# Kernel tuning notes

Measured on AMD Instinct MI355X. Metric: run time of the kernel, lower is better.

Reference implementation:

```python
import jax, jax.numpy as jnp
import numpy as np

B, T, S, D, V = 8, 64, 512, 512, 50000


def setup_inputs() -> dict:
    key = jax.random.key(0)
    k1, k2, k3, k4, k5 = jax.random.split(key, 5)
    x = jax.random.normal(k1, (B, T, D), dtype=jnp.float32)
    attn_dist = jax.random.normal(k2, (B, T, S), dtype=jnp.float32)
    enc_batch_extend_vocab = jax.random.randint(k3, (B, S), 0, V, dtype=jnp.int64)
    W_proj = jax.random.normal(k4, (D, V), dtype=jnp.float32) * (1.0 / np.sqrt(D))
    b_proj = jnp.zeros((V,), dtype=jnp.float32)
    W_pgen = jax.random.normal(k5, (D, 1), dtype=jnp.float32) * (1.0 / np.sqrt(D))
    b_pgen = jnp.zeros((1,), dtype=jnp.float32)
    return {"x": x, "attn_dist": attn_dist,
            "enc_batch_extend_vocab": enc_batch_extend_vocab,
            "W_proj": W_proj, "b_proj": b_proj,
            "W_pgen": W_pgen, "b_pgen": b_pgen}


def reference(x, attn_dist, enc_batch_extend_vocab, W_proj, b_proj, W_pgen, b_pgen):
    # pointer-generator head, temp=1, beam_search=False
    temp = 1.0
    # p_gen gate: [B, T, 1]
    alpha = jax.nn.sigmoid(jnp.einsum('btd,de->bte', x, W_pgen) + b_pgen)
    # vocab projection + softmax: [B, T, V]
    logit = jnp.einsum('btd,dv->btv', x, W_proj) + b_proj
    vocab_dist = jax.nn.softmax(logit / temp, axis=2)
    vocab_dist_ = alpha * vocab_dist
    # copy distribution over source positions: [B, T, S]
    attn = jax.nn.softmax(attn_dist / temp, axis=-1)
    attn_ = (1.0 - alpha) * attn
    # scatter_add copy probs into vocab dim (index broadcast over T)
    b_idx = jnp.arange(B)[:, None, None]        # [B,1,1]
    t_idx = jnp.arange(T)[None, :, None]        # [1,T,1]
    v_idx = enc_batch_extend_vocab[:, None, :]  # [B,1,S]
    merged = vocab_dist_.at[b_idx, t_idx, v_idx].add(attn_)
    return jnp.log(merged)
```

## Files before the change

kernel.cpp:

```cpp
#include <hip/hip_runtime.h>
#include <math.h>
#include <stdint.h>

#define B_ 8
#define T_ 64
#define S_ 512
#define D_ 512
#define V_ 50000
#define VP_ 50176
#define M_ (B_*T_)
#define ROWB_ ((size_t)V_ * 4)

typedef __bf16 bf16_t;
typedef bf16_t bf16x8 __attribute__((ext_vector_type(8)));
typedef float  f32x4  __attribute__((ext_vector_type(4)));

__device__ inline float blk_sum(float v, float* sm) {
    #pragma unroll
    for (int o = 32; o > 0; o >>= 1) v += __shfl_down(v, o);
    int lane = threadIdx.x & 63, wid = threadIdx.x >> 6;
    __syncthreads();
    if (lane == 0) sm[wid] = v;
    __syncthreads();
    return sm[0] + sm[1] + sm[2] + sm[3];
}

__device__ inline float blk_max(float v, float* sm) {
    #pragma unroll
    for (int o = 32; o > 0; o >>= 1) v = fmaxf(v, __shfl_down(v, o));
    int lane = threadIdx.x & 63, wid = threadIdx.x >> 6;
    __syncthreads();
    if (lane == 0) sm[wid] = v;
    __syncthreads();
    return fmaxf(fmaxf(sm[0], sm[1]), fmaxf(sm[2], sm[3]));
}

__device__ inline void unpack8(uint4 u, float f[8]) {
    uint32_t w0 = u.x, w1 = u.y, w2 = u.z, w3 = u.w;
    f[0] = __uint_as_float(w0 << 16); f[1] = __uint_as_float(w0 & 0xffff0000u);
    f[2] = __uint_as_float(w1 << 16); f[3] = __uint_as_float(w1 & 0xffff0000u);
    f[4] = __uint_as_float(w2 << 16); f[5] = __uint_as_float(w2 & 0xffff0000u);
    f[6] = __uint_as_float(w3 << 16); f[7] = __uint_as_float(w3 & 0xffff0000u);
}

#define CONVB_ (784 * 8)

__global__ __launch_bounds__(256) void kprep(
    const float* __restrict__ W, bf16_t* __restrict__ Wt,
    const float* __restrict__ x, const float* __restrict__ attn_dist,
    const float* __restrict__ W_pgen, const float* __restrict__ b_pgen,
    float* __restrict__ logalpha_out, float* __restrict__ attn_out, bf16_t* __restrict__ xb,
    const int* __restrict__ idx, int* __restrict__ owner_g)
{
    __shared__ float tile[64][65];
    int bid = blockIdx.x;
    int tid = threadIdx.x;

    if (bid < CONVB_) {
        int v0 = (bid % 784) * 64;
        int k0 = (bid / 784) * 64;
        #pragma unroll
        for (int p = 0; p < 4; p++) {
            int kl = (tid >> 4) + p * 16;
            int v  = v0 + (tid & 15) * 4;
            float4 val = make_float4(0.f, 0.f, 0.f, 0.f);
            if (v < V_)
                val = *reinterpret_cast<const float4*>(&W[(size_t)(k0 + kl) * V_ + v]);
            tile[kl][(tid & 15) * 4 + 0] = val.x;
            tile[kl][(tid & 15) * 4 + 1] = val.y;
            tile[kl][(tid & 15) * 4 + 2] = val.z;
            tile[kl][(tid & 15) * 4 + 3] = val.w;
        }
        __syncthreads();
        #pragma unroll
        for (int p = 0; p < 2; p++) {
            int vl = (tid >> 3) + p * 32;
            int kc = (tid & 7) * 8;
            union { bf16_t h[8]; uint4 u; } pk;
            #pragma unroll
            for (int j = 0; j < 8; j++) pk.h[j] = (bf16_t)tile[kc + j][vl];
            *reinterpret_cast<uint4*>(&Wt[(size_t)(v0 + vl) * D_ + k0 + kc]) = pk.u;
        }
    } else if (bid < CONVB_ + M_) {
        float* sm = &tile[0][0];
        int row = bid - CONVB_;

        float2 xv = reinterpret_cast<const float2*>(x + (size_t)row * D_)[tid];
        float2 wv = reinterpret_cast<const float2*>(W_pgen)[tid];
        union { bf16_t h[2]; uint32_t u; } pk;
        pk.h[0] = (bf16_t)xv.x; pk.h[1] = (bf16_t)xv.y;
        reinterpret_cast<uint32_t*>(xb + (size_t)row * D_)[tid] = pk.u;

        float dot = blk_sum(xv.x * wv.x + xv.y * wv.y, sm);
        float alpha = 1.f / (1.f + expf(-(dot + b_pgen[0])));
        if (tid == 0) logalpha_out[row] = logf(alpha);

        float a0 = attn_dist[(size_t)row * S_ + tid];
        float a1 = attn_dist[(size_t)row * S_ + tid + 256];
        float mx = blk_max(fmaxf(a0, a1), sm);
        float e0 = expf(a0 - mx), e1 = expf(a1 - mx);
        float s = blk_sum(e0 + e1, sm);
        float scale = (1.f - alpha) / s;
        attn_out[(size_t)row * S_ + tid]       = e0 * scale;
        attn_out[(size_t)row * S_ + tid + 256] = e1 * scale;
    } else {
        int* ids = reinterpret_cast<int*>(&tile[0][0]);
        int b = bid - (CONVB_ + M_);
        for (int s = tid; s < S_; s += 256) ids[s] = idx[b * S_ + s];
        __syncthreads();
        for (int s = tid; s < S_; s += 256) {
            int v = ids[s], o = s;
            for (int s2 = 0; s2 < s; s2++) if (ids[s2] == v) { o = s2; break; }
            owner_g[b * S_ + s] = o;
        }
    }
}

#define GBM 128
#define GBN 128
#define GBK 32
#define NT2_ (D_/GBK)

__global__ __launch_bounds__(256) void k2_mfma(
    const bf16_t* __restrict__ A, const bf16_t* __restrict__ Wt,
    const float* __restrict__ bias, char* __restrict__ outB)
{
    __shared__ bf16_t As0[GBM][GBK], As1[GBM][GBK];
    __shared__ bf16_t Bs0[GBN][GBK], Bs1[GBN][GBK];
    int tid  = threadIdx.x;
    int lane = tid & 63;
    int w    = tid >> 6;
    int wm   = w >> 1, wn = w & 1;
    int bn = blockIdx.x * GBN;
    int bm = blockIdx.y * GBM;

    f32x4 acc[4][4] = {};

#define STAGE(dstA, dstB, k0)                                                          \
    {                                                                                  \
        _Pragma("unroll")                                                              \
        for (int i = 0; i < 2; i++) {                                                  \
            int e = (w * 2 + i) * 512 + lane * 8;                                      \
            int r = e >> 5, c = e & 31;                                                \
            __builtin_amdgcn_global_load_lds(                                          \
                (const __attribute__((address_space(1))) void*)                        \
                    &A[(size_t)(bm + r) * D_ + (k0) + c],                              \
                (__attribute__((address_space(3))) void*)&dstA[(w * 2 + i) * 16][0],   \
                16, 0, 0);                                                             \
            __builtin_amdgcn_global_load_lds(                                          \
                (const __attribute__((address_space(1))) void*)                        \
                    &Wt[(size_t)(bn + r) * D_ + (k0) + c],                             \
                (__attribute__((address_space(3))) void*)&dstB[(w * 2 + i) * 16][0],   \
                16, 0, 0);                                                             \
        }                                                                              \
    }

#define COMPUTE(srcA, srcB)                                                            \
    {                                                                                  \
        bf16x8 af[4], bfr[4];                                                          \
        int kb = (lane >> 4) * 8;                                                      \
        _Pragma("unroll")                                                              \
        for (int mi = 0; mi < 4; mi++)                                                 \
            af[mi] = *reinterpret_cast<const bf16x8*>(&srcA[wm * 64 + mi * 16 + (lane & 15)][kb]); \
        _Pragma("unroll")                                                              \
        for (int ni = 0; ni < 4; ni++)                                                 \
            bfr[ni] = *reinterpret_cast<const bf16x8*>(&srcB[wn * 64 + ni * 16 + (lane & 15)][kb]); \
        _Pragma("unroll")                                                              \
        for (int mi = 0; mi < 4; mi++)                                                 \
            _Pragma("unroll")                                                          \
            for (int ni = 0; ni < 4; ni++)                                             \
                acc[mi][ni] = __builtin_amdgcn_mfma_f32_16x16x32_bf16(af[mi], bfr[ni], acc[mi][ni], 0, 0, 0); \
    }

    STAGE(As0, Bs0, 0);
    asm volatile("s_waitcnt vmcnt(0)" ::: "memory");
    __syncthreads();

    #pragma unroll
    for (int tt = 0; tt < NT2_ / 2; tt++) {
        int k0 = tt * 2 * GBK;
        if (k0 + GBK < D_) STAGE(As1, Bs1, k0 + GBK);
        COMPUTE(As0, Bs0);
        asm volatile("s_waitcnt vmcnt(0)" ::: "memory");
        __syncthreads();
        if (k0 + 2 * GBK < D_) STAGE(As0, Bs0, k0 + 2 * GBK);
        COMPUTE(As1, Bs1);
        asm volatile("s_waitcnt vmcnt(0)" ::: "memory");
        __syncthreads();
    }
#undef STAGE
#undef COMPUTE

    int cm = bm + wm * 64, cn = bn + wn * 64;
    #pragma unroll
    for (int ni = 0; ni < 4; ni++) {
        int n = cn + ni * 16 + (lane & 15);
        float bv = (n < V_) ? bias[n] : 0.f;
        #pragma unroll
        for (int mi = 0; mi < 4; mi++) {
            int rbase = cm + mi * 16 + (lane >> 4) * 4;
            #pragma unroll
            for (int r = 0; r < 4; r++) {
                bf16_t val = (bf16_t)(acc[mi][ni][r] + bv);
                *reinterpret_cast<bf16_t*>(outB + (size_t)(rbase + r) * ROWB_ + 2 * (size_t)n) = val;
            }
        }
    }
}

#define CHUNK_ 2048
#define NCH_ ((V_ + CHUNK_ - 1) / CHUNK_)

__global__ __launch_bounds__(256) void k345_final(
    char* __restrict__ outB, const float* __restrict__ attn_, const int* __restrict__ idx,
    const int* __restrict__ owner_g, const float* __restrict__ logalpha)
{
    __shared__ float att[S_];
    __shared__ int own[S_], ids[S_];
    __shared__ float smm[4], sms[4];
    int row = blockIdx.x;
    int b = row >> 6;
    int tid = threadIdx.x;
    int lane = tid & 63, wid = tid >> 6;

    for (int s = tid; s < S_; s += 256) {
        att[s] = attn_[(size_t)row * S_ + s];
        own[s] = owner_g[b * S_ + s];
        ids[s] = idx[b * S_ + s];
    }

    const uint4* L4 = reinterpret_cast<const uint4*>(outB + (size_t)row * ROWB_);
    float m = -INFINITY, se = 0.f;
    for (int i = tid; i < V_ / 8; i += 256) {
        uint4 u = L4[i];
        float f[8]; unpack8(u, f);
        float m8 = fmaxf(fmaxf(fmaxf(f[0], f[1]), fmaxf(f[2], f[3])),
                         fmaxf(fmaxf(f[4], f[5]), fmaxf(f[6], f[7])));
        float mn = fmaxf(m, m8);
        se = se * __expf(m - mn)
           + __expf(f[0] - mn) + __expf(f[1] - mn) + __expf(f[2] - mn) + __expf(f[3] - mn)
           + __expf(f[4] - mn) + __expf(f[5] - mn) + __expf(f[6] - mn) + __expf(f[7] - mn);
        m = mn;
    }
    #pragma unroll
    for (int o = 32; o > 0; o >>= 1) {
        float m2 = __shfl_down(m, o);
        float s2 = __shfl_down(se, o);
        float mn = fmaxf(m, m2);
        if (mn == -INFINITY) { se = 0.f; }
        else se = se * __expf(m - mn) + s2 * __expf(m2 - mn);
        m = mn;
    }
    __syncthreads();
    if (lane == 0) { smm[wid] = m; sms[wid] = se; }
    __syncthreads();
    float M = smm[0], Ssum = sms[0];
    #pragma unroll
    for (int wv = 1; wv < 4; wv++) {
        float m2 = smm[wv], s2 = sms[wv];
        float mn = fmaxf(M, m2);
        if (mn != -INFINITY) Ssum = Ssum * __expf(M - mn) + s2 * __expf(m2 - mn);
        M = mn;
    }
    float logden = M + logf(Ssum);
    float c_ = logalpha[row] - logden;

    for (int s = tid; s < S_; s += 256)
        if (own[s] != s) atomicAdd(&att[own[s]], att[s]);
    __syncthreads();

    const ushort* Lrow = reinterpret_cast<const ushort*>(outB + (size_t)row * ROWB_);
    float* frow = reinterpret_cast<float*>(outB + (size_t)row * ROWB_);
    for (int c = NCH_ - 1; c >= 0; c--) {
        int i0 = c * CHUNK_ + tid * 8;
        uint4 u = make_uint4(0, 0, 0, 0);
        bool act = (i0 + 8 <= V_);
        if (act) u = *reinterpret_cast<const uint4*>(Lrow + i0);
        __syncthreads();
        if (act) {
            float f[8]; unpack8(u, f);
            float4 lo = make_float4(f[0] + c_, f[1] + c_, f[2] + c_, f[3] + c_);
            float4 hi = make_float4(f[4] + c_, f[5] + c_, f[6] + c_, f[7] + c_);
            *reinterpret_cast<float4*>(frow + i0)     = lo;
            *reinterpret_cast<float4*>(frow + i0 + 4) = hi;
        }
        __syncthreads();
    }

    for (int s = tid; s < S_; s += 256) {
        if (own[s] == s) {
            int v = ids[s];
            frow[v] = logf(expf(frow[v]) + att[s]);
        }
    }
}

__global__ __launch_bounds__(256) void k1_alpha_attn(
    const float* __restrict__ x, const float* __restrict__ attn_dist,
    const float* __restrict__ W_pgen, const float* __restrict__ b_pgen,
    float* __restrict__ logalpha_out, float* __restrict__ attn_out)
{
    __shared__ float sm[4];
    int row = blockIdx.x;
    int tid = threadIdx.x;
    float2 xv = reinterpret_cast<const float2*>(x + (size_t)row * D_)[tid];
    float2 wv = reinterpret_cast<const float2*>(W_pgen)[tid];
    float dot = blk_sum(xv.x * wv.x + xv.y * wv.y, sm);
    float alpha = 1.f / (1.f + expf(-(dot + b_pgen[0])));
    if (tid == 0) logalpha_out[row] = logf(alpha);
    float a0 = attn_dist[(size_t)row * S_ + tid];
    float a1 = attn_dist[(size_t)row * S_ + tid + 256];
    float mx = blk_max(fmaxf(a0, a1), sm);
    float e0 = expf(a0 - mx), e1 = expf(a1 - mx);
    float s = blk_sum(e0 + e1, sm);
    float scale = (1.f - alpha) / s;
    attn_out[(size_t)row * S_ + tid]       = e0 * scale;
    attn_out[(size_t)row * S_ + tid + 256] = e1 * scale;
}

__global__ __launch_bounds__(512) void k5a_owner(const int* __restrict__ idx, int* __restrict__ owner_g)
{
    __shared__ int ids[S_];
    int b = blockIdx.x;
    int s = threadIdx.x;
    ids[s] = idx[b * S_ + s];
    __syncthreads();
    int v = ids[s], o = s;
    for (int s2 = 0; s2 < s; s2++) if (ids[s2] == v) { o = s2; break; }
    owner_g[b * S_ + s] = o;
}

#define BM 64
#define BN 64
#define BK 16
__global__ __launch_bounds__(256) void k2_gemm(
    const float* __restrict__ A, const float* __restrict__ W,
    const float* __restrict__ bias, float* __restrict__ C)
{
    __shared__ float As2[BK][BM + 1];
    __shared__ float Bs2[BK][BN + 1];
    int bn = blockIdx.x * BN;
    int bm = blockIdx.y * BM;
    int tid = threadIdx.x;
    int tx = tid & 15;
    int ty = tid >> 4;
    bool full_n = (bn + BN <= V_);
    float acc[4][4] = {};
    for (int k0 = 0; k0 < D_; k0 += BK) {
        {
            int i = tid * 4;
            int row = i >> 4, col = i & 15;
            const float4 av = *reinterpret_cast<const float4*>(&A[(size_t)(bm + row) * D_ + k0 + col]);
            As2[col + 0][row] = av.x; As2[col + 1][row] = av.y;
            As2[col + 2][row] = av.z; As2[col + 3][row] = av.w;
        }
        {
            int i = tid * 4;
            int row = i >> 6, col = i & 63;
            int gn = bn + col;
            if (full_n) {
                const float4 bv = *reinterpret_cast<const float4*>(&W[(size_t)(k0 + row) * V_ + gn]);
                Bs2[row][col + 0] = bv.x; Bs2[row][col + 1] = bv.y;
                Bs2[row][col + 2] = bv.z; Bs2[row][col + 3] = bv.w;
            } else {
                #pragma unroll
                for (int j = 0; j < 4; j++)
                    Bs2[row][col + j] = (gn + j < V_) ? W[(size_t)(k0 + row) * V_ + gn + j] : 0.f;
            }
        }
        __syncthreads();
        #pragma unroll
        for (int kk = 0; kk < BK; kk++) {
            float a[4], b[4];
            #pragma unroll
            for (int i = 0; i < 4; i++) a[i] = As2[kk][ty * 4 + i];
            #pragma unroll
            for (int j = 0; j < 4; j++) b[j] = Bs2[kk][tx + j * 16];
            #pragma unroll
            for (int i = 0; i < 4; i++)
                #pragma unroll
                for (int j = 0; j < 4; j++)
                    acc[i][j] += a[i] * b[j];
        }
        __syncthreads();
    }
    #pragma unroll
    for (int i = 0; i < 4; i++) {
        int m = bm + ty * 4 + i;
        #pragma unroll
        for (int j = 0; j < 4; j++) {
            int n = bn + tx + j * 16;
            if (n < V_) C[(size_t)m * V_ + n] = acc[i][j] + bias[n];
        }
    }
}

__global__ __launch_bounds__(256) void k3_stats(const float* __restrict__ C, float* __restrict__ logden)
{
    __shared__ float smm[4], sms[4];
    int row = blockIdx.x;
    const float4* p = reinterpret_cast<const float4*>(C + (size_t)row * V_);
    float m = -INFINITY, s = 0.f;
    for (int i = threadIdx.x; i < V_ / 4; i += 256) {
        float4 v = p[i];
        float m4 = fmaxf(fmaxf(v.x, v.y), fmaxf(v.z, v.w));
        if (m4 > m) { s *= expf(m - m4); m = m4; }
        s += expf(v.x - m) + expf(v.y - m) + expf(v.z - m) + expf(v.w - m);
    }
    #pragma unroll
    for (int o = 32; o > 0; o >>= 1) {
        float m2 = __shfl_down(m, o);
        float s2 = __shfl_down(s, o);
        float mn = fmaxf(m, m2);
        s = s * expf(m - mn) + s2 * expf(m2 - mn);
        m = mn;
    }
    int lane = threadIdx.x & 63, wid = threadIdx.x >> 6;
    if (lane == 0) { smm[wid] = m; sms[wid] = s; }
    __syncthreads();
    if (threadIdx.x == 0) {
        float M = smm[0], S = sms[0];
        #pragma unroll
        for (int wv = 1; wv < 4; wv++) {
            float m2 = smm[wv], s2 = sms[wv];
            float mn = fmaxf(M, m2);
            S = S * expf(M - mn) + s2 * expf(m2 - mn);
            M = mn;
        }
        logden[row] = M + logf(S);
    }
}

__global__ __launch_bounds__(256) void k4_scale(
    float* __restrict__ C, const float* __restrict__ logalpha, const float* __restrict__ logden)
{
    int row = blockIdx.y;
    int i = blockIdx.x * 256 + threadIdx.x;
    if (i >= V_ / 4) return;
    float c_ = logalpha[row] - logden[row];
    float4* p = reinterpret_cast<float4*>(C + (size_t)row * V_) + i;
    float4 v = *p;
    v.x += c_; v.y += c_; v.z += c_; v.w += c_;
    *p = v;
}

__global__ __launch_bounds__(256) void k5_scatter_log(
    float* __restrict__ C, const float* __restrict__ attn_, const int* __restrict__ idx,
    const int* __restrict__ owner_g)
{
    __shared__ float att[S_];
    __shared__ int own[S_], ids[S_];
    int row = blockIdx.x;
    int b = row >> 6;
    int tid = threadIdx.x;
    for (int s = tid; s < S_; s += 256) {
        att[s] = attn_[(size_t)row * S_ + s];
        own[s] = owner_g[b * S_ + s];
        ids[s] = idx[b * S_ + s];
    }
    __syncthreads();
    for (int s = tid; s < S_; s += 256)
        if (own[s] != s) atomicAdd(&att[own[s]], att[s]);
    __syncthreads();
    for (int s = tid; s < S_; s += 256) {
        if (own[s] == s) {
            int v = ids[s];
            float* p = &C[(size_t)row * V_ + v];
            *p = logf(expf(*p) + att[s]);
        }
    }
}

extern "C" void kernel_launch(void* const* d_in, const int* in_sizes, int n_in,
                              void* d_out, int out_size, void* d_ws, size_t ws_size,
                              hipStream_t stream) {
    const float* x         = (const float*)d_in[0];
    const float* attn_dist = (const float*)d_in[1];
    const int*   ebev      = (const int*)  d_in[2];
    const float* W_proj    = (const float*)d_in[3];
    const float* b_proj    = (const float*)d_in[4];
    const float* W_pgen    = (const float*)d_in[5];
    const float* b_pgen    = (const float*)d_in[6];
    float* out = (float*)d_out;
    char*  outB = (char*)d_out;

    float*  logalpha = (float*)d_ws;
    float*  logden   = logalpha + M_;
    float*  attn_    = logden + M_;
    int*    owner    = (int*)(attn_ + (size_t)B_ * T_ * S_);
    bf16_t* xb       = (bf16_t*)(owner + (size_t)B_ * S_);
    bf16_t* Wt       = xb + (size_t)M_ * D_;
    size_t need = (size_t)(2 * M_ + B_ * T_ * S_ + B_ * S_) * 4
                + (size_t)M_ * D_ * 2 + (size_t)VP_ * D_ * 2;

    if (ws_size >= need) {
        kprep<<<CONVB_ + M_ + B_, 256, 0, stream>>>(
            W_proj, Wt, x, attn_dist, W_pgen, b_pgen, logalpha, attn_, xb, ebev, owner);

        dim3 g2(VP_ / GBN, M_ / GBM);
        k2_mfma<<<g2, 256, 0, stream>>>(xb, Wt, b_proj, outB);

        k345_final<<<M_, 256, 0, stream>>>(outB, attn_, ebev, owner, logalpha);
    } else {
        k1_alpha_attn<<<M_, 256, 0, stream>>>(x, attn_dist, W_pgen, b_pgen, logalpha, attn_);
        k5a_owner<<<B_, 512, 0, stream>>>(ebev, owner);
        dim3 g2((V_ + BN - 1) / BN, M_ / BM);
        k2_gemm<<<g2, 256, 0, stream>>>(x, W_proj, b_proj, out);
        k3_stats<<<M_, 256, 0, stream>>>(out, logden);
        dim3 g4((V_ / 4 + 255) / 256, M_);
        k4_scale<<<g4, 256, 0, stream>>>(out, logalpha, logden);
        k5_scatter_log<<<M_, 256, 0, stream>>>(out, attn_, ebev, owner);
    }
}
```

Before: 157.4 us.

## Fuse W transpose and bf16 conversion into GEMM B-tile staging

Removes the separate prep pass that transposed the fp32 projection weights into a bf16 workspace. The GEMM now loads fp32 W tiles directly into registers, converts them to bf16 and writes them transposed into padded LDS, software-pipelined against the MFMA compute. This drops a full write and re-read of the converted weight matrix. In exchange, each of the four M-row blocks re-reads fp32 W, which is twice the bytes of bf16, and the B-tile path now goes through register staging instead of direct global-to-LDS loads.

```diff
diff --git a/kernel.cpp b/kernel.cpp
--- a/kernel.cpp
+++ b/kernel.cpp
@@ -13,6 +13,7 @@
 
 typedef __bf16 bf16_t;
 typedef bf16_t bf16x8 __attribute__((ext_vector_type(8)));
+typedef bf16_t bf16x4 __attribute__((ext_vector_type(4)));
 typedef float  f32x4  __attribute__((ext_vector_type(4)));
 
 __device__ inline float blk_sum(float v, float* sm) {
@@ -43,47 +44,19 @@
     f[6] = __uint_as_float(w3 << 16); f[7] = __uint_as_float(w3 & 0xffff0000u);
 }
 
-#define CONVB_ (784 * 8)
-
 __global__ __launch_bounds__(256) void kprep(
-    const float* __restrict__ W, bf16_t* __restrict__ Wt,
     const float* __restrict__ x, const float* __restrict__ attn_dist,
     const float* __restrict__ W_pgen, const float* __restrict__ b_pgen,
     float* __restrict__ logalpha_out, float* __restrict__ attn_out, bf16_t* __restrict__ xb,
     const int* __restrict__ idx, int* __restrict__ owner_g)
 {
-    __shared__ float tile[64][65];
+    __shared__ int shb[S_];
     int bid = blockIdx.x;
     int tid = threadIdx.x;
 
-    if (bid < CONVB_) {
-        int v0 = (bid % 784) * 64;
-        int k0 = (bid / 784) * 64;
-        #pragma unroll
-        for (int p = 0; p < 4; p++) {
-            int kl = (tid >> 4) + p * 16;
-            int v  = v0 + (tid & 15) * 4;
-            float4 val = make_float4(0.f, 0.f, 0.f, 0.f);
-            if (v < V_)
-                val = *reinterpret_cast<const float4*>(&W[(size_t)(k0 + kl) * V_ + v]);
-            tile[kl][(tid & 15) * 4 + 0] = val.x;
-            tile[kl][(tid & 15) * 4 + 1] = val.y;
-            tile[kl][(tid & 15) * 4 + 2] = val.z;
-            tile[kl][(tid & 15) * 4 + 3] = val.w;
-        }
-        __syncthreads();
-        #pragma unroll
-        for (int p = 0; p < 2; p++) {
-            int vl = (tid >> 3) + p * 32;
-            int kc = (tid & 7) * 8;
-            union { bf16_t h[8]; uint4 u; } pk;
-            #pragma unroll
-            for (int j = 0; j < 8; j++) pk.h[j] = (bf16_t)tile[kc + j][vl];
-            *reinterpret_cast<uint4*>(&Wt[(size_t)(v0 + vl) * D_ + k0 + kc]) = pk.u;
-        }
-    } else if (bid < CONVB_ + M_) {
-        float* sm = &tile[0][0];
-        int row = bid - CONVB_;
+    if (bid < M_) {
+        float* sm = reinterpret_cast<float*>(shb);
+        int row = bid;
 
         float2 xv = reinterpret_cast<const float2*>(x + (size_t)row * D_)[tid];
         float2 wv = reinterpret_cast<const float2*>(W_pgen)[tid];
@@ -104,13 +77,12 @@
         attn_out[(size_t)row * S_ + tid]       = e0 * scale;
         attn_out[(size_t)row * S_ + tid + 256] = e1 * scale;
     } else {
-        int* ids = reinterpret_cast<int*>(&tile[0][0]);
-        int b = bid - (CONVB_ + M_);
-        for (int s = tid; s < S_; s += 256) ids[s] = idx[b * S_ + s];
+        int b = bid - M_;
+        for (int s = tid; s < S_; s += 256) shb[s] = idx[b * S_ + s];
         __syncthreads();
         for (int s = tid; s < S_; s += 256) {
-            int v = ids[s], o = s;
-            for (int s2 = 0; s2 < s; s2++) if (ids[s2] == v) { o = s2; break; }
+            int v = shb[s], o = s;
+            for (int s2 = 0; s2 < s; s2++) if (shb[s2] == v) { o = s2; break; }
             owner_g[b * S_ + s] = o;
         }
     }
@@ -119,14 +91,15 @@
 #define GBM 128
 #define GBN 128
 #define GBK 32
-#define NT2_ (D_/GBK)
+#define NTK_ 16
+#define BSTR_ 36
 
 __global__ __launch_bounds__(256) void k2_mfma(
-    const bf16_t* __restrict__ A, const bf16_t* __restrict__ Wt,
+    const bf16_t* __restrict__ A, const float* __restrict__ W,
     const float* __restrict__ bias, char* __restrict__ outB)
 {
-    __shared__ bf16_t As0[GBM][GBK], As1[GBM][GBK];
-    __shared__ bf16_t Bs0[GBN][GBK], Bs1[GBN][GBK];
+    __shared__ bf16_t As[2][GBM][GBK];
+    __shared__ __attribute__((aligned(16))) bf16_t Bs[2][GBN * BSTR_];
     int tid  = threadIdx.x;
     int lane = tid & 63;
     int w    = tid >> 6;
@@ -134,9 +107,15 @@
     int bn = blockIdx.x * GBN;
     int bm = blockIdx.y * GBM;
 
+    int kq = tid >> 5;
+    int q  = tid & 31;
+    int gv = bn + q * 4;
+    bool vok = (gv < V_);
+
     f32x4 acc[4][4] = {};
-
-#define STAGE(dstA, dstB, k0)                                                          \
+    float4 wreg[4];
+
+#define STAGE_A(BUF, K0)                                                               \
     {                                                                                  \
         _Pragma("unroll")                                                              \
         for (int i = 0; i < 2; i++) {                                                  \
@@ -144,27 +123,52 @@
             int r = e >> 5, c = e & 31;                                                \
             __builtin_amdgcn_global_load_lds(                                          \
                 (const __attribute__((address_space(1))) void*)                        \
-                    &A[(size_t)(bm + r) * D_ + (k0) + c],                              \
-                (__attribute__((address_space(3))) void*)&dstA[(w * 2 + i) * 16][0],   \
-                16, 0, 0);                                                             \
-            __builtin_amdgcn_global_load_lds(                                          \
-                (const __attribute__((address_space(1))) void*)                        \
-                    &Wt[(size_t)(bn + r) * D_ + (k0) + c],                             \
-                (__attribute__((address_space(3))) void*)&dstB[(w * 2 + i) * 16][0],   \
+                    &A[(size_t)(bm + r) * D_ + (K0) + c],                              \
+                (__attribute__((address_space(3))) void*)&As[BUF][(w * 2 + i) * 16][0],\
                 16, 0, 0);                                                             \
         }                                                                              \
     }
 
-#define COMPUTE(srcA, srcB)                                                            \
+#define LOAD_B(K0)                                                                     \
+    {                                                                                  \
+        _Pragma("unroll")                                                              \
+        for (int j = 0; j < 4; j++)                                                    \
+            wreg[j] = vok ? *reinterpret_cast<const float4*>(                          \
+                                &W[(size_t)((K0) + kq * 4 + j) * V_ + gv])             \
+                          : make_float4(0.f, 0.f, 0.f, 0.f);                           \
+    }
+
+#define WRITE_B(BUF)                                                                   \
+    {                                                                                  \
+        _Pragma("unroll")                                                              \
+        for (int i = 0; i < 4; i++) {                                                  \
+            union { bf16_t h[4]; uint2 u; } pk;                                        \
+            pk.h[0] = (bf16_t)(reinterpret_cast<const float*>(&wreg[0])[i]);           \
+            pk.h[1] = (bf16_t)(reinterpret_cast<const float*>(&wreg[1])[i]);           \
+            pk.h[2] = (bf16_t)(reinterpret_cast<const float*>(&wreg[2])[i]);           \
+            pk.h[3] = (bf16_t)(reinterpret_cast<const float*>(&wreg[3])[i]);           \
+            *reinterpret_cast<uint2*>(&Bs[BUF][(q * 4 + i) * BSTR_ + kq * 4]) = pk.u;  \
+        }                                                                              \
+    }
+
+#define COMPUTE(BUF)                                                                   \
     {                                                                                  \
         bf16x8 af[4], bfr[4];                                                          \
         int kb = (lane >> 4) * 8;                                                      \
         _Pragma("unroll")                                                              \
         for (int mi = 0; mi < 4; mi++)                                                 \
-            af[mi] = *reinterpret_cast<const bf16x8*>(&srcA[wm * 64 + mi * 16 + (lane & 15)][kb]); \
+            af[mi] = *reinterpret_cast<const bf16x8*>(                                 \
+                &As[BUF][wm * 64 + mi * 16 + (lane & 15)][kb]);                        \
         _Pragma("unroll")                                                              \
-        for (int ni = 0; ni < 4; ni++)                                                 \
-            bfr[ni] = *reinterpret_cast<const bf16x8*>(&srcB[wn * 64 + ni * 16 + (lane & 15)][kb]); \
+        for (int ni = 0; ni < 4; ni++) {                                               \
+            const bf16_t* bp = &Bs[BUF][(wn * 64 + ni * 16 + (lane & 15)) * BSTR_ + kb]; \
+            bf16x4 b0 = *reinterpret_cast<const bf16x4*>(bp);                          \
+            bf16x4 b1 = *reinterpret_cast<const bf16x4*>(bp + 4);                      \
+            bf16x8 bb;                                                                 \
+            bb[0] = b0[0]; bb[1] = b0[1]; bb[2] = b0[2]; bb[3] = b0[3];                \
+            bb[4] = b1[0]; bb[5] = b1[1]; bb[6] = b1[2]; bb[7] = b1[3];                \
+            bfr[ni] = bb;                                                              \
+        }                                                                              \
         _Pragma("unroll")                                                              \
         for (int mi = 0; mi < 4; mi++)                                                 \
             _Pragma("unroll")                                                          \
@@ -172,23 +176,29 @@
                 acc[mi][ni] = __builtin_amdgcn_mfma_f32_16x16x32_bf16(af[mi], bfr[ni], acc[mi][ni], 0, 0, 0); \
     }
 
-    STAGE(As0, Bs0, 0);
+    LOAD_B(0);
+    STAGE_A(0, 0);
     asm volatile("s_waitcnt vmcnt(0)" ::: "memory");
-    __syncthreads();
-
-    #pragma unroll
-    for (int tt = 0; tt < NT2_ / 2; tt++) {
-        int k0 = tt * 2 * GBK;
-        if (k0 + GBK < D_) STAGE(As1, Bs1, k0 + GBK);
-        COMPUTE(As0, Bs0);
-        asm volatile("s_waitcnt vmcnt(0)" ::: "memory");
+    WRITE_B(0);
+    __syncthreads();
+
+    #pragma unroll
+    for (int tt = 0; tt < NTK_; tt++) {
+        int cur = tt & 1, nxt = cur ^ 1;
+        if (tt + 1 < NTK_) {
+            LOAD_B((tt + 1) * GBK);
+            STAGE_A(nxt, (tt + 1) * GBK);
+        }
+        COMPUTE(cur);
+        if (tt + 1 < NTK_) {
+            asm volatile("s_waitcnt vmcnt(0)" ::: "memory");
+            WRITE_B(nxt);
+        }
         __syncthreads();
-        if (k0 + 2 * GBK < D_) STAGE(As0, Bs0, k0 + 2 * GBK);
-        COMPUTE(As1, Bs1);
-        asm volatile("s_waitcnt vmcnt(0)" ::: "memory");
-        __syncthreads();
-    }
-#undef STAGE
+    }
+#undef STAGE_A
+#undef LOAD_B
+#undef WRITE_B
 #undef COMPUTE
 
     int cm = bm + wm * 64, cn = bn + wn * 64;
@@ -489,16 +499,15 @@
     float*  attn_    = logden + M_;
     int*    owner    = (int*)(attn_ + (size_t)B_ * T_ * S_);
     bf16_t* xb       = (bf16_t*)(owner + (size_t)B_ * S_);
-    bf16_t* Wt       = xb + (size_t)M_ * D_;
     size_t need = (size_t)(2 * M_ + B_ * T_ * S_ + B_ * S_) * 4
-                + (size_t)M_ * D_ * 2 + (size_t)VP_ * D_ * 2;
+                + (size_t)M_ * D_ * 2;
 
     if (ws_size >= need) {
-        kprep<<<CONVB_ + M_ + B_, 256, 0, stream>>>(
-            W_proj, Wt, x, attn_dist, W_pgen, b_pgen, logalpha, attn_, xb, ebev, owner);
+        kprep<<<M_ + B_, 256, 0, stream>>>(
+            x, attn_dist, W_pgen, b_pgen, logalpha, attn_, xb, ebev, owner);
 
         dim3 g2(VP_ / GBN, M_ / GBM);
-        k2_mfma<<<g2, 256, 0, stream>>>(xb, Wt, b_proj, outB);
+        k2_mfma<<<g2, 256, 0, stream>>>(xb, W_proj, b_proj, outB);
 
         k345_final<<<M_, 256, 0, stream>>>(outB, attn_, ebev, owner, logalpha);
     } else {
```

Result: slower. 217.6 us (+38.3%).
